# Kernel tuning notes

Hardware: AMD Instinct MI355X
Metric: run time of the kernel (lower is better)

The kernel has to match this reference:

```python
import jax, jax.numpy as jnp
import numpy as np
import math

DIM_PER_HEAD = 64

def setup_inputs() -> dict:
    key = jax.random.key(0)
    k1, k2, k3, k4 = jax.random.split(key, 4)
    B, H, S, D = 2, 16, 2048, 64
    mat1 = jax.random.normal(k1, (B, H, S, D), dtype=jnp.float32)
    mat2 = jax.random.normal(k2, (B, H, S, D), dtype=jnp.float32)
    mat3 = jax.random.normal(k3, (B, H, S, D), dtype=jnp.float32)
    bias = jax.random.normal(k4, (1, 1, S, S), dtype=jnp.float32)
    return {"mat1": mat1, "mat2": mat2, "mat3": mat3, "bias": bias}

def reference(mat1, mat2, mat3, bias) -> jnp.ndarray:
    # scale Q, scores = QK^T + bias, softmax over last dim, then @ V
    scale = 1.0 / math.sqrt(DIM_PER_HEAD)
    qk = jnp.einsum('bhqd,bhkd->bhqk', mat1 * scale, mat2)  # [B,H,S,S]
    scores = jax.nn.softmax(qk + bias, axis=-1)
    return jnp.einsum('bhqk,bhkd->bhqd', scores, mat3)
```

## Files before the change

### kernel.cpp

```cpp
#include <hip/hip_runtime.h>
#include <hip/hip_bf16.h>


#define SEQ 2048
#define DH  64
#define BHN 32
#define NTILE (SEQ / 64)
#define LOG2E 1.44269504088896f

typedef __attribute__((ext_vector_type(8))) short bf16x8;
typedef __attribute__((ext_vector_type(4))) float f32x4;
typedef __attribute__((ext_vector_type(8))) short short8v;

__device__ inline short f2b(float x) {
    union { float f; unsigned u; } v; v.f = x;
    unsigned r = v.u + 0x7fff + ((v.u >> 16) & 1);
    return (short)(r >> 16);
}

__device__ inline void gl_lds16(const void* g, void* l) {
    __builtin_amdgcn_global_load_lds(
        (const __attribute__((address_space(1))) void*)g,
        (__attribute__((address_space(3))) void*)l, 16, 0, 0);
}

__global__ __launch_bounds__(256)
void prep_kv(const float* __restrict__ K, const float* __restrict__ V,
             short* __restrict__ Kb, short* __restrict__ Vt) {
    __shared__ short t[64 * 72];
    const int tid = threadIdx.x;
    const int bh = blockIdx.x >> 5, st = blockIdx.x & 31, s0 = st * 64;

    {
        const float* Kp = K + ((size_t)bh * SEQ + s0) * DH;
        short* Ko = Kb + ((size_t)bh * SEQ + s0) * DH;
        #pragma unroll
        for (int i = 0; i < 2; ++i) {
            size_t o = (size_t)(tid + i * 256) * 8;
            f32x4 a = *(const f32x4*)(Kp + o);
            f32x4 b = *(const f32x4*)(Kp + o + 4);
            short8v s;
            #pragma unroll
            for (int j = 0; j < 4; ++j) { s[j] = f2b(a[j]); s[4 + j] = f2b(b[j]); }
            *(short8v*)(Ko + o) = s;
        }
    }

    const float* Vb = V + (size_t)bh * SEQ * DH + (size_t)s0 * DH;
    #pragma unroll
    for (int i = 0; i < 4; ++i) {
        int c = tid + i * 256, s = c >> 4, c4 = c & 15;
        f32x4 v = *(const f32x4*)(Vb + s * DH + c4 * 4);
        #pragma unroll
        for (int j = 0; j < 4; ++j) t[s * 72 + c4 * 4 + j] = f2b(v[j]);
    }
    __syncthreads();
    const int d = tid >> 2, part = tid & 3;
    short8v lo, hi;
    #pragma unroll
    for (int j = 0; j < 8; ++j) {
        lo[j] = t[(part * 16 + j) * 72 + d];
        hi[j] = t[(part * 16 + 8 + j) * 72 + d];
    }
    short* outp = Vt + (size_t)bh * DH * SEQ + (size_t)d * SEQ + s0 + part * 16;
    *(short8v*)outp = lo;
    *(short8v*)(outp + 8) = hi;
}

__global__ __launch_bounds__(256, 4)
void mha_main(const float* __restrict__ Q, const float* __restrict__ Bias,
              const short* __restrict__ Kb, const short* __restrict__ Vt,
              float* __restrict__ Out)
{
    __shared__ short lds_k[2][64 * DH];
    __shared__ short lds_v[2][64 * DH];
    __shared__ short lds_p[4 * 16 * 64];

    const int tid = threadIdx.x, lane = tid & 63, wave = tid >> 6;
    const int l15 = lane & 15, l4 = lane >> 4;
    const int qb = blockIdx.x & 31, bh = blockIdx.x >> 5;
    const int q0 = qb * 64;

    const float* Qb = Q + (size_t)bh * SEQ * DH;
    const short* Kh = Kb + (size_t)bh * SEQ * DH;
    const short* Vh = Vt + (size_t)bh * DH * SEQ;
    float* Ob = Out + (size_t)bh * SEQ * DH;

    bf16x8 qf[2];
    {
        const float* qp = Qb + (size_t)(q0 + wave * 16 + l15) * DH;
        const float qs = 0.125f * LOG2E;
        #pragma unroll
        for (int ks = 0; ks < 2; ++ks) {
            short tmp[8];
            #pragma unroll
            for (int j = 0; j < 8; ++j) tmp[j] = f2b(qp[ks * 32 + l4 * 8 + j] * qs);
            qf[ks] = *reinterpret_cast<bf16x8*>(tmp);
        }
    }

    f32x4 o_acc[4];
    #pragma unroll
    for (int dt = 0; dt < 4; ++dt) o_acc[dt] = f32x4{0.f, 0.f, 0.f, 0.f};
    float l_part[4] = {0.f, 0.f, 0.f, 0.f};

    const short* kg[2]; const short* vg[2]; short* kl[2]; short* vl[2];
    #pragma unroll
    for (int p = 0; p < 2; ++p) {
        int slot = p * 256 + wave * 64 + lane;
        int r_ = slot >> 3;
        int c_ = slot & 7;
        int cg = c_ ^ (r_ & 7);
        kg[p] = Kh + (size_t)r_ * DH + cg * 8;
        vg[p] = Vh + (size_t)r_ * SEQ + cg * 8;
        kl[p] = &lds_k[0][(size_t)(p * 256 + wave * 64) * 8];
        vl[p] = &lds_v[0][(size_t)(p * 256 + wave * 64) * 8];
    }
    const float* bp0 = Bias + (size_t)(q0 + wave * 16 + l4 * 4) * SEQ + l15;
    short* pw = &lds_p[wave * 16 * 64];
    const int swz = l15 & 7;

    gl_lds16(kg[0], kl[0]);
    gl_lds16(kg[1], kl[1]);
    gl_lds16(vg[0], vl[0]);
    gl_lds16(vg[1], vl[1]);

    float bpre[4][4];
    #pragma unroll
    for (int nt = 0; nt < 4; ++nt)
        #pragma unroll
        for (int r = 0; r < 4; ++r)
            bpre[nt][r] = bp0[(size_t)r * SEQ + nt * 16];

    __syncthreads();

    for (int kt = 0; kt < NTILE; ++kt) {
        const int cur = kt & 1;
        const int nb = cur ^ 1;

        if (kt + 1 < NTILE) {
            const size_t koff = (size_t)(kt + 1) * 64 * DH;
            const int voff = (kt + 1) * 64;
            const int lo = nb * (64 * DH);
            gl_lds16(kg[0] + koff, kl[0] + lo);
            gl_lds16(kg[1] + koff, kl[1] + lo);
            gl_lds16(vg[0] + voff, vl[0] + lo);
            gl_lds16(vg[1] + voff, vl[1] + lo);
        }

        f32x4 sacc[4];
        #pragma unroll
        for (int nt = 0; nt < 4; ++nt)
            #pragma unroll
            for (int r = 0; r < 4; ++r)
                sacc[nt][r] = bpre[nt][r] * LOG2E;

        if (kt + 1 < NTILE) {
            const float* bp = bp0 + (kt + 1) * 64;
            #pragma unroll
            for (int nt = 0; nt < 4; ++nt)
                #pragma unroll
                for (int r = 0; r < 4; ++r)
                    bpre[nt][r] = bp[(size_t)r * SEQ + nt * 16];
        }

        const short* lk = lds_k[cur];
        const short* lv = lds_v[cur];

        #pragma unroll
        for (int ks = 0; ks < 2; ++ks)
            #pragma unroll
            for (int nt = 0; nt < 4; ++nt) {
                int cc = (ks * 4 + l4) ^ swz;
                bf16x8 kf = *(const bf16x8*)&lk[(nt * 16 + l15) * DH + cc * 8];
                sacc[nt] = __builtin_amdgcn_mfma_f32_16x16x32_bf16(qf[ks], kf, sacc[nt], 0, 0, 0);
            }

        #pragma unroll
        for (int r = 0; r < 4; ++r) {
            const int prow = l4 * 4 + r;
            const int rsw = prow & 7;
            #pragma unroll
            for (int nt = 0; nt < 4; ++nt) {
                float pv = __builtin_amdgcn_exp2f(sacc[nt][r]);
                l_part[r] += pv;
                int pc = (nt * 2 + (l15 >> 3)) ^ rsw;
                pw[prow * 64 + pc * 8 + (l15 & 7)] = f2b(pv);
            }
        }

        #pragma unroll
        for (int ks = 0; ks < 2; ++ks) {
            int cc = (ks * 4 + l4) ^ swz;
            bf16x8 pf = *(const bf16x8*)&pw[l15 * 64 + cc * 8];
            #pragma unroll
            for (int dt = 0; dt < 4; ++dt) {
                bf16x8 vf = *(const bf16x8*)&lv[(dt * 16 + l15) * DH + cc * 8];
                o_acc[dt] = __builtin_amdgcn_mfma_f32_16x16x32_bf16(pf, vf, o_acc[dt], 0, 0, 0);
            }
        }

        __syncthreads();
    }

    #pragma unroll
    for (int r = 0; r < 4; ++r) {
        float s = l_part[r];
        #pragma unroll
        for (int m = 1; m < 16; m <<= 1) s += __shfl_xor(s, m, 64);
        l_part[r] = s;
    }

    #pragma unroll
    for (int r = 0; r < 4; ++r) {
        float inv = 1.0f / l_part[r];
        float* op = Ob + (size_t)(q0 + wave * 16 + l4 * 4 + r) * DH + l15;
        #pragma unroll
        for (int dt = 0; dt < 4; ++dt) op[dt * 16] = o_acc[dt][r] * inv;
    }
}

extern "C" void kernel_launch(void* const* d_in, const int* in_sizes, int n_in,
                              void* d_out, int out_size, void* d_ws, size_t ws_size,
                              hipStream_t stream) {
    const float* Q    = (const float*)d_in[0];
    const float* K    = (const float*)d_in[1];
    const float* V    = (const float*)d_in[2];
    const float* Bias = (const float*)d_in[3];
    float* O          = (float*)d_out;

    short* Kb = (short*)d_ws;
    short* Vt = Kb + (size_t)BHN * SEQ * DH;

    prep_kv<<<dim3(BHN * 32), dim3(256), 0, stream>>>(K, V, Kb, Vt);
    mha_main<<<dim3(BHN * 32), dim3(256), 0, stream>>>(Q, Bias, Kb, Vt, O);
}
```

Before: 169.4 us.

## Switch attention to 32x32x16 MFMA with transposed S and register-resident P

Moves the main attention kernel from 16x16x32 to 32x32x16 bf16 MFMA. S is computed transposed (K as the A operand), so each lane holds a column of scores, and the P operand for the PV product is built in registers via packed bf16 conversion and a cross-half lane shuffle instead of a round trip through LDS. Each block now covers 128 query rows (32 per wave), halving the grid and doubling K/V reuse per LDS load. Bias loads become vectorized f32x4 and s_setprio wraps the MFMA sections. The trade-off is higher register pressure (launch bounds relaxed to 2 blocks per SIMD-target) and fewer blocks in flight.

```diff
diff --git a/kernel.cpp b/kernel.cpp
--- a/kernel.cpp
+++ b/kernel.cpp
@@ -10,12 +10,19 @@
 
 typedef __attribute__((ext_vector_type(8))) short bf16x8;
 typedef __attribute__((ext_vector_type(4))) float f32x4;
+typedef __attribute__((ext_vector_type(16))) float f32x16;
 typedef __attribute__((ext_vector_type(8))) short short8v;
 
 __device__ inline short f2b(float x) {
     union { float f; unsigned u; } v; v.f = x;
     unsigned r = v.u + 0x7fff + ((v.u >> 16) & 1);
     return (short)(r >> 16);
+}
+
+__device__ inline unsigned cvt_pk(float lo, float hi) {
+    unsigned r;
+    asm("v_cvt_pk_bf16_f32 %0, %1, %2" : "=v"(r) : "v"(lo), "v"(hi));
+    return r;
 }
 
 __device__ inline void gl_lds16(const void* g, void* l) {
@@ -67,70 +74,72 @@
     *(short8v*)(outp + 8) = hi;
 }
 
-__global__ __launch_bounds__(256, 4)
+__global__ __launch_bounds__(256, 2)
 void mha_main(const float* __restrict__ Q, const float* __restrict__ Bias,
               const short* __restrict__ Kb, const short* __restrict__ Vt,
               float* __restrict__ Out)
 {
     __shared__ short lds_k[2][64 * DH];
     __shared__ short lds_v[2][64 * DH];
-    __shared__ short lds_p[4 * 16 * 64];
 
     const int tid = threadIdx.x, lane = tid & 63, wave = tid >> 6;
-    const int l15 = lane & 15, l4 = lane >> 4;
-    const int qb = blockIdx.x & 31, bh = blockIdx.x >> 5;
-    const int q0 = qb * 64;
+    const int c = lane & 31, h = lane >> 5;
+    const int qb = blockIdx.x & 15, bh = blockIdx.x >> 4;
+    const int q0 = qb * 128 + wave * 32;
 
     const float* Qb = Q + (size_t)bh * SEQ * DH;
     const short* Kh = Kb + (size_t)bh * SEQ * DH;
     const short* Vh = Vt + (size_t)bh * DH * SEQ;
     float* Ob = Out + (size_t)bh * SEQ * DH;
 
-    bf16x8 qf[2];
+    bf16x8 qf[4];
     {
-        const float* qp = Qb + (size_t)(q0 + wave * 16 + l15) * DH;
+        const float* qp = Qb + (size_t)(q0 + c) * DH;
         const float qs = 0.125f * LOG2E;
         #pragma unroll
-        for (int ks = 0; ks < 2; ++ks) {
+        for (int ks = 0; ks < 4; ++ks) {
+            f32x4 x = *(const f32x4*)(qp + ks * 16 + h * 8);
+            f32x4 y = *(const f32x4*)(qp + ks * 16 + h * 8 + 4);
             short tmp[8];
             #pragma unroll
-            for (int j = 0; j < 8; ++j) tmp[j] = f2b(qp[ks * 32 + l4 * 8 + j] * qs);
+            for (int j = 0; j < 4; ++j) { tmp[j] = f2b(x[j] * qs); tmp[4 + j] = f2b(y[j] * qs); }
             qf[ks] = *reinterpret_cast<bf16x8*>(tmp);
         }
     }
 
-    f32x4 o_acc[4];
-    #pragma unroll
-    for (int dt = 0; dt < 4; ++dt) o_acc[dt] = f32x4{0.f, 0.f, 0.f, 0.f};
-    float l_part[4] = {0.f, 0.f, 0.f, 0.f};
+    f32x16 o_acc[2];
+    #pragma unroll
+    for (int dt = 0; dt < 2; ++dt)
+        #pragma unroll
+        for (int i = 0; i < 16; ++i) o_acc[dt][i] = 0.f;
+    float l_acc[4] = {0.f, 0.f, 0.f, 0.f};
 
     const short* kg[2]; const short* vg[2]; short* kl[2]; short* vl[2];
     #pragma unroll
     for (int p = 0; p < 2; ++p) {
-        int slot = p * 256 + wave * 64 + lane;
+        int slot = p * 256 + tid;
         int r_ = slot >> 3;
         int c_ = slot & 7;
         int cg = c_ ^ (r_ & 7);
         kg[p] = Kh + (size_t)r_ * DH + cg * 8;
         vg[p] = Vh + (size_t)r_ * SEQ + cg * 8;
-        kl[p] = &lds_k[0][(size_t)(p * 256 + wave * 64) * 8];
-        vl[p] = &lds_v[0][(size_t)(p * 256 + wave * 64) * 8];
-    }
-    const float* bp0 = Bias + (size_t)(q0 + wave * 16 + l4 * 4) * SEQ + l15;
-    short* pw = &lds_p[wave * 16 * 64];
-    const int swz = l15 & 7;
+        kl[p] = &lds_k[0][(size_t)slot * 8];
+        vl[p] = &lds_v[0][(size_t)slot * 8];
+    }
+    const float* bp0 = Bias + (size_t)(q0 + c) * SEQ;
+    const int swz = c & 7;
 
     gl_lds16(kg[0], kl[0]);
     gl_lds16(kg[1], kl[1]);
     gl_lds16(vg[0], vl[0]);
     gl_lds16(vg[1], vl[1]);
 
-    float bpre[4][4];
-    #pragma unroll
-    for (int nt = 0; nt < 4; ++nt)
-        #pragma unroll
-        for (int r = 0; r < 4; ++r)
-            bpre[nt][r] = bp0[(size_t)r * SEQ + nt * 16];
+    f32x4 bpre[2][4];
+    #pragma unroll
+    for (int nt = 0; nt < 2; ++nt)
+        #pragma unroll
+        for (int g = 0; g < 4; ++g)
+            bpre[nt][g] = *(const f32x4*)(bp0 + nt * 32 + g * 8 + h * 4);
 
     __syncthreads();
 
@@ -148,76 +157,96 @@
             gl_lds16(vg[1] + voff, vl[1] + lo);
         }
 
-        f32x4 sacc[4];
-        #pragma unroll
-        for (int nt = 0; nt < 4; ++nt)
-            #pragma unroll
-            for (int r = 0; r < 4; ++r)
-                sacc[nt][r] = bpre[nt][r] * LOG2E;
+        f32x16 sacc[2];
+        #pragma unroll
+        for (int nt = 0; nt < 2; ++nt)
+            #pragma unroll
+            for (int g = 0; g < 4; ++g)
+                #pragma unroll
+                for (int r = 0; r < 4; ++r)
+                    sacc[nt][4 * g + r] = bpre[nt][g][r] * LOG2E;
 
         if (kt + 1 < NTILE) {
             const float* bp = bp0 + (kt + 1) * 64;
             #pragma unroll
-            for (int nt = 0; nt < 4; ++nt)
-                #pragma unroll
-                for (int r = 0; r < 4; ++r)
-                    bpre[nt][r] = bp[(size_t)r * SEQ + nt * 16];
+            for (int nt = 0; nt < 2; ++nt)
+                #pragma unroll
+                for (int g = 0; g < 4; ++g)
+                    bpre[nt][g] = *(const f32x4*)(bp + nt * 32 + g * 8 + h * 4);
         }
 
         const short* lk = lds_k[cur];
         const short* lv = lds_v[cur];
 
-        #pragma unroll
-        for (int ks = 0; ks < 2; ++ks)
-            #pragma unroll
-            for (int nt = 0; nt < 4; ++nt) {
-                int cc = (ks * 4 + l4) ^ swz;
-                bf16x8 kf = *(const bf16x8*)&lk[(nt * 16 + l15) * DH + cc * 8];
-                sacc[nt] = __builtin_amdgcn_mfma_f32_16x16x32_bf16(qf[ks], kf, sacc[nt], 0, 0, 0);
+        __builtin_amdgcn_s_setprio(1);
+        #pragma unroll
+        for (int ks = 0; ks < 4; ++ks)
+            #pragma unroll
+            for (int nt = 0; nt < 2; ++nt) {
+                int row = nt * 32 + c;
+                int chunk = (2 * ks + h) ^ swz;
+                bf16x8 kf = *(const bf16x8*)&lk[row * DH + chunk * 8];
+                sacc[nt] = __builtin_amdgcn_mfma_f32_32x32x16_bf16(kf, qf[ks], sacc[nt], 0, 0, 0);
             }
-
+        __builtin_amdgcn_s_setprio(0);
+
+        #pragma unroll
+        for (int nt = 0; nt < 2; ++nt) {
+            float p[16];
+            #pragma unroll
+            for (int g = 0; g < 4; ++g)
+                #pragma unroll
+                for (int r = 0; r < 4; ++r) {
+                    float pv = __builtin_amdgcn_exp2f(sacc[nt][4 * g + r]);
+                    p[4 * g + r] = pv;
+                    l_acc[r] += pv;
+                }
+
+            #pragma unroll
+            for (int ks = 0; ks < 2; ++ks) {
+                unsigned a  = cvt_pk(p[8 * ks + 0], p[8 * ks + 1]);
+                unsigned b  = cvt_pk(p[8 * ks + 2], p[8 * ks + 3]);
+                unsigned cc = cvt_pk(p[8 * ks + 4], p[8 * ks + 5]);
+                unsigned dd = cvt_pk(p[8 * ks + 6], p[8 * ks + 7]);
+                unsigned u1 = h ? a : cc;
+                unsigned u2 = h ? b : dd;
+                unsigned r1 = __shfl_xor(u1, 32, 64);
+                unsigned r2 = __shfl_xor(u2, 32, 64);
+                union { unsigned w[4]; bf16x8 v; } pk_;
+                pk_.w[0] = h ? r1 : a;
+                pk_.w[1] = h ? r2 : b;
+                pk_.w[2] = h ? cc : r1;
+                pk_.w[3] = h ? dd : r2;
+                bf16x8 pf = pk_.v;
+
+                __builtin_amdgcn_s_setprio(1);
+                #pragma unroll
+                for (int dt = 0; dt < 2; ++dt) {
+                    int row = dt * 32 + c;
+                    int chunk = (4 * nt + 2 * ks + h) ^ swz;
+                    bf16x8 vf = *(const bf16x8*)&lv[row * DH + chunk * 8];
+                    o_acc[dt] = __builtin_amdgcn_mfma_f32_32x32x16_bf16(pf, vf, o_acc[dt], 0, 0, 0);
+                }
+                __builtin_amdgcn_s_setprio(0);
+            }
+        }
+
+        __syncthreads();
+    }
+
+    float lsum = (l_acc[0] + l_acc[1]) + (l_acc[2] + l_acc[3]);
+    lsum += __shfl_xor(lsum, 32, 64);
+    float linv = 1.0f / lsum;
+
+    #pragma unroll
+    for (int g = 0; g < 4; ++g)
         #pragma unroll
         for (int r = 0; r < 4; ++r) {
-            const int prow = l4 * 4 + r;
-            const int rsw = prow & 7;
-            #pragma unroll
-            for (int nt = 0; nt < 4; ++nt) {
-                float pv = __builtin_amdgcn_exp2f(sacc[nt][r]);
-                l_part[r] += pv;
-                int pc = (nt * 2 + (l15 >> 3)) ^ rsw;
-                pw[prow * 64 + pc * 8 + (l15 & 7)] = f2b(pv);
-            }
-        }
-
-        #pragma unroll
-        for (int ks = 0; ks < 2; ++ks) {
-            int cc = (ks * 4 + l4) ^ swz;
-            bf16x8 pf = *(const bf16x8*)&pw[l15 * 64 + cc * 8];
-            #pragma unroll
-            for (int dt = 0; dt < 4; ++dt) {
-                bf16x8 vf = *(const bf16x8*)&lv[(dt * 16 + l15) * DH + cc * 8];
-                o_acc[dt] = __builtin_amdgcn_mfma_f32_16x16x32_bf16(pf, vf, o_acc[dt], 0, 0, 0);
-            }
-        }
-
-        __syncthreads();
-    }
-
-    #pragma unroll
-    for (int r = 0; r < 4; ++r) {
-        float s = l_part[r];
-        #pragma unroll
-        for (int m = 1; m < 16; m <<= 1) s += __shfl_xor(s, m, 64);
-        l_part[r] = s;
-    }
-
-    #pragma unroll
-    for (int r = 0; r < 4; ++r) {
-        float inv = 1.0f / l_part[r];
-        float* op = Ob + (size_t)(q0 + wave * 16 + l4 * 4 + r) * DH + l15;
-        #pragma unroll
-        for (int dt = 0; dt < 4; ++dt) op[dt * 16] = o_acc[dt][r] * inv;
-    }
+            float inv = __shfl(linv, r + 8 * g + 4 * h, 64);
+            float* op = Ob + (size_t)(q0 + r + 8 * g + 4 * h) * DH + c;
+            op[0]  = o_acc[0][4 * g + r] * inv;
+            op[32] = o_acc[1][4 * g + r] * inv;
+        }
 }
 
 extern "C" void kernel_launch(void* const* d_in, const int* in_sizes, int n_in,
@@ -233,5 +262,5 @@
     short* Vt = Kb + (size_t)BHN * SEQ * DH;
 
     prep_kv<<<dim3(BHN * 32), dim3(256), 0, stream>>>(K, V, Kb, Vt);
-    mha_main<<<dim3(BHN * 32), dim3(256), 0, stream>>>(Q, Bias, Kb, Vt, O);
-}
+    mha_main<<<dim3(BHN * 16), dim3(256), 0, stream>>>(Q, Bias, Kb, Vt, O);
+}
```

New measurement: 176.1 us. 1.04x slower.
